# Performance work log

Hardware: AMD Instinct MI355X
Metric: run time of the kernel (lower is better)

## Reference

```python
import jax, jax.numpy as jnp
import numpy as np

B, T, C = 128, 256, 384
H, D = 6, 64

def setup_inputs() -> dict:
    key = jax.random.key(0)
    ks = jax.random.split(key, 6)
    s = 1.0 / np.sqrt(C)
    return {
        "x": jax.random.normal(ks[0], (B, T, C), dtype=jnp.float32),
        "Wq": jax.random.normal(ks[1], (H, C, D), dtype=jnp.float32) * s,
        "Wk": jax.random.normal(ks[2], (H, C, D), dtype=jnp.float32) * s,
        "Wv": jax.random.normal(ks[3], (H, C, D), dtype=jnp.float32) * s,
        "Wp": jax.random.normal(ks[4], (C, C), dtype=jnp.float32) * s,
        "bp": jnp.zeros((C,), dtype=jnp.float32),
    }

def reference(x, Wq, Wk, Wv, Wp, bp):
    # per-head projections (all heads at once): [B,T,C] x [H,C,D] -> [B,H,T,D]
    q = jnp.einsum("btc,hcd->bhtd", x, Wq)
    k = jnp.einsum("btc,hcd->bhtd", x, Wk)
    v = jnp.einsum("btc,hcd->bhtd", x, Wv)
    scale = 1.0 / jnp.sqrt(jnp.asarray(D, dtype=x.dtype))
    # scores [B,H,T,T], causal mask, softmax
    wei = jnp.einsum("bhqd,bhkd->bhqk", q, k) * scale
    causal = jnp.tril(jnp.ones((T, T), dtype=bool))
    wei = jnp.where(causal, wei, -jnp.inf)
    wei = jax.nn.softmax(wei, axis=-1)
    # dropout layers are identity in eval mode
    out = jnp.einsum("bhqk,bhkd->bhqd", wei, v)
    # concat heads: [B,T,H*D]
    out = out.transpose(0, 2, 1, 3).reshape(B, T, H * D)
    return out @ Wp + bp
```

## Files before the change

### kernel.cpp

```cpp
#include <hip/hip_runtime.h>
#include <stdint.h>


typedef __attribute__((ext_vector_type(8))) short bf16x8;
typedef __attribute__((ext_vector_type(4))) float f32x4;
typedef __attribute__((ext_vector_type(16))) float f32x16;

__device__ __forceinline__ unsigned short f2b(float f) {
    union { float f; unsigned int u; } v; v.f = f;
    unsigned int u = v.u + 0x7fffu + ((v.u >> 16) & 1u);
    return (unsigned short)(u >> 16);
}

__device__ __forceinline__ unsigned int pk2(float lo, float hi) {
    return (unsigned int)f2b(lo) | ((unsigned int)f2b(hi) << 16);
}

__device__ __forceinline__ uint32_t cvtpk(float lo, float hi) {
    uint32_t r;
    asm("v_cvt_pk_bf16_f32 %0, %1, %2" : "=v"(r) : "v"(lo), "v"(hi));
    return r;
}

__device__ __forceinline__ void gload_lds16(const void* g, void* lds) {
    auto gp = reinterpret_cast<const __attribute__((address_space(1))) uint32_t*>(
        reinterpret_cast<uintptr_t>(g));
    auto lp = reinterpret_cast<__attribute__((address_space(3))) uint32_t*>(
        reinterpret_cast<uintptr_t>(lds));
    __builtin_amdgcn_global_load_lds(gp, lp, 16, 0, 0);
}

#define SBAR0() __builtin_amdgcn_sched_barrier(0)


__global__ void cvt_w_kernel(const float* __restrict__ Wq, const float* __restrict__ Wk,
                             const float* __restrict__ Wv, const float* __restrict__ Wp,
                             unsigned short* __restrict__ wt, unsigned short* __restrict__ wpt) {
    int i = blockIdx.x * 256 + threadIdx.x;
    if (i >= 589824) return;
    if (i < 442368) {
        int j = i / 384, c = i - j * 384;
        int p = j / 384, rem = j - p * 384;
        int h = rem >> 6, d = rem & 63;
        const float* W = (p == 0) ? Wq : ((p == 1) ? Wk : Wv);
        wt[i] = f2b(W[(size_t)(h * 384 + c) * 64 + d]);
    } else {
        int i2 = i - 442368;
        int n = i2 / 384, c = i2 - n * 384;
        wpt[i2] = f2b(Wp[(size_t)c * 384 + n]);
    }
}


__global__ __launch_bounds__(256, 2) void gemm_qkv(
    const float* __restrict__ x,
    const unsigned short* __restrict__ wt,
    unsigned short* __restrict__ qO,
    unsigned short* __restrict__ kO,
    unsigned short* __restrict__ vO)
{
    extern __shared__ __align__(16) unsigned short smem[];
    float*          Af = (float*)smem;
    unsigned short* Bf = smem + 24576;

    const int tid  = threadIdx.x;
    const int lane = tid & 63;
    const int w    = tid >> 6;
    const int wm = w >> 1, wn = w & 1;

    const int flat = blockIdx.y * 9 + blockIdx.x;
    const int swz = (flat & 7) * 288 + (flat >> 3);
    const int bx = swz % 9, by = swz / 9;
    const int col0 = bx * 128;
    const int row0 = by * 128;

    const float* Abase = x + (size_t)row0 * 384;
    const unsigned short* Bbase = wt + (size_t)col0 * 384;

    f32x4 acc[4][4];
#pragma unroll
    for (int mf = 0; mf < 4; ++mf)
#pragma unroll
        for (int nf = 0; nf < 4; ++nf)
#pragma unroll
            for (int r = 0; r < 4; ++r) acc[mf][nf][r] = 0.f;

    const float* aSrc[4];
#pragma unroll
    for (int j = 0; j < 4; ++j) {
        const int ci = tid + 256 * j;
        aSrc[j] = Abase + (size_t)(ci >> 3) * 384 + ((ci & 7) ^ ((ci >> 3) & 7)) * 4;
    }
    const int bi0 = tid, bi1 = tid + 256;
    const unsigned short* bSrc0 = Bbase + (size_t)(bi0 >> 2) * 384 + ((bi0 & 3) ^ ((bi0 >> 3) & 3)) * 8;
    const unsigned short* bSrc1 = Bbase + (size_t)(bi1 >> 2) * 384 + ((bi1 & 3) ^ ((bi1 >> 3) & 3)) * 8;
    const int cb = w * 64;

    auto STAGE = [&](int buf, int kt) {
        const int k0_ = kt * 32;
#pragma unroll
        for (int j = 0; j < 4; ++j)
            gload_lds16(aSrc[j] + k0_, Af + buf * 4096 + (cb + 256 * j) * 4);
        gload_lds16(bSrc0 + k0_, Bf + buf * 4096 + (cb + 0) * 8);
        gload_lds16(bSrc1 + k0_, Bf + buf * 4096 + (cb + 256) * 8);
    };

    const int fr  = lane & 15;
    const int oc  = lane >> 4;
    const int qlA0 = (2 * oc)     ^ (fr & 7);
    const int qlA1 = (2 * oc + 1) ^ (fr & 7);
    const int ocB  = oc ^ ((fr >> 1) & 3);

    auto COMPUTE = [&](int buf) {
        const float* A = Af + buf * 4096;
        const unsigned short* B = Bf + buf * 4096;
        bf16x8 aF[4], bF[4];
#pragma unroll
        for (int mf = 0; mf < 4; ++mf) {
            const int rowA = wm * 64 + mf * 16 + fr;
            f32x4 F0 = *(const f32x4*)&A[rowA * 32 + qlA0 * 4];
            f32x4 F1 = *(const f32x4*)&A[rowA * 32 + qlA1 * 4];
            union { uint32_t u[4]; bf16x8 v; } pk;
            pk.u[0] = cvtpk(F0[0], F0[1]);
            pk.u[1] = cvtpk(F0[2], F0[3]);
            pk.u[2] = cvtpk(F1[0], F1[1]);
            pk.u[3] = cvtpk(F1[2], F1[3]);
            aF[mf] = pk.v;
        }
#pragma unroll
        for (int nf = 0; nf < 4; ++nf)
            bF[nf] = *(const bf16x8*)&B[(wn * 64 + nf * 16 + fr) * 32 + ocB * 8];
#pragma unroll
        for (int mf = 0; mf < 4; ++mf)
#pragma unroll
            for (int nf = 0; nf < 4; ++nf)
                acc[mf][nf] = __builtin_amdgcn_mfma_f32_16x16x32_bf16(aF[mf], bF[nf], acc[mf][nf], 0, 0, 0);
    };

    STAGE(0, 0);
    STAGE(1, 1);
    SBAR0();
    int bufS = 2, bufC = 0;
    for (int t = 0; t < 10; ++t) {
        STAGE(bufS, t + 2);
        bufS = (bufS == 2) ? 0 : bufS + 1;
        SBAR0();
        asm volatile("s_waitcnt vmcnt(12)" ::: "memory");
        SBAR0();
        __builtin_amdgcn_s_barrier();
        SBAR0();
        COMPUTE(bufC);
        bufC = (bufC == 2) ? 0 : bufC + 1;
        SBAR0();
        __builtin_amdgcn_s_barrier();
        SBAR0();
    }
    asm volatile("s_waitcnt vmcnt(6)" ::: "memory");
    SBAR0();
    __builtin_amdgcn_s_barrier();
    SBAR0();
    COMPUTE(1);
    SBAR0();
    __builtin_amdgcn_s_barrier();
    SBAR0();
    asm volatile("s_waitcnt vmcnt(0)" ::: "memory");
    SBAR0();
    __builtin_amdgcn_s_barrier();
    SBAR0();
    COMPUTE(2);
    __syncthreads();

    unsigned short* Ct = smem;
    const int co = tid & 15;
    const int rr = tid >> 4;
    const int colg = col0 + co * 8;
    const int p = colg / 384;
    const int rem = colg - p * 384;
    const int h = rem >> 6;
    const int d = rem & 63;
    unsigned short* dst = (p == 0) ? qO : ((p == 1) ? kO : vO);

#pragma unroll
    for (int ph = 0; ph < 2; ++ph) {
        if (wm == ph) {
#pragma unroll
            for (int mf = 0; mf < 4; ++mf)
#pragma unroll
                for (int nf = 0; nf < 4; ++nf)
#pragma unroll
                    for (int r = 0; r < 4; ++r)
                        Ct[(mf * 16 + (lane >> 4) * 4 + r) * 136 + wn * 64 + nf * 16 + (lane & 15)] =
                            f2b(acc[mf][nf][r]);
        }
        __syncthreads();
#pragma unroll
        for (int it = 0; it < 4; ++it) {
            const int r_loc = it * 16 + rr;
            const int m = row0 + ph * 64 + r_loc;
            const int b = m >> 8, t = m & 255;
            uint4 val = *(const uint4*)&Ct[r_loc * 136 + co * 8];
            *(uint4*)&dst[(size_t)((b * 6 + h) * 256 + t) * 64 + d] = val;
        }
        __syncthreads();
    }
}


__global__ __launch_bounds__(512, 4) void attn_kernel(
    const unsigned short* __restrict__ Qg,
    const unsigned short* __restrict__ Kg,
    const unsigned short* __restrict__ Vg,
    unsigned short* __restrict__ Og)
{
    extern __shared__ __align__(16) unsigned short asmem[];
    unsigned short* Ks = asmem;
    unsigned short* Vs = asmem + 256 * 72;
    unsigned short* Ot = asmem;
    const int bh = blockIdx.x;
    const int b = bh / 6, h = bh - b * 6;
    const int tid = threadIdx.x;
    const int lane = tid & 63;
    const int w = tid >> 6;
    const int lo = lane & 31, hi = lane >> 5;

    const unsigned short* kg = Kg + (size_t)bh * 256 * 64;
#pragma unroll
    for (int j = 0; j < 4; ++j) {
        int chunk = tid + 512 * j;
        int key = chunk >> 3, dc = (chunk & 7) * 8;
        *(uint4*)&Ks[key * 72 + dc] = *(const uint4*)&kg[key * 64 + dc];
    }
    {
        const unsigned short* vg = Vg + (size_t)bh * 256 * 64;
        uint32_t* Vs32 = (uint32_t*)Vs;
#pragma unroll
        for (int i = 0; i < 2; ++i) {
            int u = tid + 512 * i;
            int t2 = (u & 31) | ((u >> 8) << 5);
            int dm = (u >> 5) & 7;
            uint4 r0 = *(const uint4*)&vg[(2 * t2 + 0) * 64 + dm * 8];
            uint4 r1 = *(const uint4*)&vg[(2 * t2 + 1) * 64 + dm * 8];
            const unsigned short* e0 = (const unsigned short*)&r0;
            const unsigned short* e1 = (const unsigned short*)&r1;
#pragma unroll
            for (int j = 0; j < 8; ++j)
                Vs32[(dm * 8 + j) * 132 + t2] = (uint32_t)e0[j] | ((uint32_t)e1[j] << 16);
        }
    }
    __syncthreads();

    const int q0 = w * 32;
    const unsigned short* qg = Qg + (size_t)bh * 256 * 64 + (size_t)(q0 + lo) * 64 + hi * 8;
    bf16x8 qF[4];
#pragma unroll
    for (int dc = 0; dc < 4; ++dc) qF[dc] = *(const bf16x8*)(qg + dc * 16);

    float m = -1e30f, ssum = 0.f;
    f32x16 o0, o1;
#pragma unroll
    for (int r = 0; r < 16; ++r) { o0[r] = 0.f; o1[r] = 0.f; }

    for (int kt = 0; kt <= w; ++kt) {
        f32x16 s;
#pragma unroll
        for (int r = 0; r < 16; ++r) s[r] = 0.f;
#pragma unroll
        for (int dc = 0; dc < 4; ++dc) {
            bf16x8 aK = *(const bf16x8*)&Ks[(kt * 32 + lo) * 72 + dc * 16 + hi * 8];
            s = __builtin_amdgcn_mfma_f32_32x32x16_bf16(aK, qF[dc], s, 0, 0, 0);
        }
        float p[16];
        float pmax = -1e30f;
        const bool diag = (kt == w);
#pragma unroll
        for (int r = 0; r < 16; ++r) {
            float sv = s[r] * 0.125f;
            const int keyl = (r & 3) + 8 * (r >> 2) + 4 * hi;
            if (diag && keyl > lo) sv = -1e30f;
            p[r] = sv;
            pmax = fmaxf(pmax, sv);
        }
        pmax = fmaxf(pmax, __shfl_xor(pmax, 32, 64));
        const float mn = fmaxf(m, pmax);
        const float sf = __expf(m - mn);
        m = mn;
        ssum *= sf;
#pragma unroll
        for (int r = 0; r < 16; ++r) { o0[r] *= sf; o1[r] *= sf; }
        float rs = 0.f;
#pragma unroll
        for (int r = 0; r < 16; ++r) { p[r] = __expf(p[r] - m); rs += p[r]; }
        rs += __shfl_xor(rs, 32, 64);
        ssum += rs;

        union { unsigned short u[16]; bf16x8 v[2]; } P;
        {
            float recv[4];
#pragma unroll
            for (int j2 = 0; j2 < 4; ++j2) {
                float sendv = hi ? p[j2] : p[4 + j2];
                recv[j2] = __shfl_xor(sendv, 32, 64);
            }
#pragma unroll
            for (int i = 0; i < 4; ++i) P.u[i]     = f2b(hi ? recv[i] : p[i]);
#pragma unroll
            for (int i = 0; i < 4; ++i) P.u[4 + i] = f2b(hi ? p[4 + i] : recv[i]);
        }
        {
            float recv[4];
#pragma unroll
            for (int j2 = 0; j2 < 4; ++j2) {
                float sendv = hi ? p[8 + j2] : p[12 + j2];
                recv[j2] = __shfl_xor(sendv, 32, 64);
            }
#pragma unroll
            for (int i = 0; i < 4; ++i) P.u[8 + i]  = f2b(hi ? recv[i] : p[8 + i]);
#pragma unroll
            for (int i = 0; i < 4; ++i) P.u[12 + i] = f2b(hi ? p[12 + i] : recv[i]);
        }

#pragma unroll
        for (int kc = 0; kc < 2; ++kc) {
            bf16x8 aV0 = *(const bf16x8*)&Vs[lo * 264 + kt * 32 + kc * 16 + hi * 8];
            o0 = __builtin_amdgcn_mfma_f32_32x32x16_bf16(aV0, P.v[kc], o0, 0, 0, 0);
            bf16x8 aV1 = *(const bf16x8*)&Vs[(32 + lo) * 264 + kt * 32 + kc * 16 + hi * 8];
            o1 = __builtin_amdgcn_mfma_f32_32x32x16_bf16(aV1, P.v[kc], o1, 0, 0, 0);
        }
    }

    __syncthreads();
    const float inv = 1.f / ssum;
    {
        uint32_t* ot32 = (uint32_t*)&Ot[w * 32 * 72];
#pragma unroll
        for (int g = 0; g < 4; ++g) {
            const int dbase0 = 8 * g + 4 * hi;
            uint32_t w0 = pk2(o0[4 * g + 0] * inv, o0[4 * g + 1] * inv);
            uint32_t w1 = pk2(o0[4 * g + 2] * inv, o0[4 * g + 3] * inv);
            int dw = lo * 36 + (dbase0 >> 1);
            ot32[dw] = w0;
            ot32[dw + 1] = w1;
            uint32_t w2 = pk2(o1[4 * g + 0] * inv, o1[4 * g + 1] * inv);
            uint32_t w3 = pk2(o1[4 * g + 2] * inv, o1[4 * g + 3] * inv);
            int dw1 = lo * 36 + ((32 + dbase0) >> 1);
            ot32[dw1] = w2;
            ot32[dw1 + 1] = w3;
        }
    }
    __syncthreads();
    {
        const unsigned short* ot = &Ot[w * 32 * 72];
        const int q = lane >> 1;
        const int half = (lane & 1) * 32;
        unsigned short* og = Og + (size_t)(b * 256 + q0 + q) * 384 + h * 64 + half;
#pragma unroll
        for (int jj = 0; jj < 4; ++jj) {
            uint4 val = *(const uint4*)&ot[q * 72 + half + jj * 8];
            *(uint4*)&og[jj * 8] = val;
        }
    }
}


__global__ __launch_bounds__(256, 3) void gemm_proj(
    const unsigned short* __restrict__ ob,
    const unsigned short* __restrict__ wpt,
    const float* __restrict__ bp,
    float* __restrict__ out)
{
    __shared__ __align__(16) unsigned short As[3][128 * 32];
    __shared__ __align__(16) unsigned short Bs[3][128 * 32];
    const int tid  = threadIdx.x;
    const int lane = tid & 63;
    const int w    = tid >> 6;
    const int wm = w >> 1, wn = w & 1;

    const int flat = blockIdx.y * 3 + blockIdx.x;
    const int swz = (flat & 7) * 96 + (flat >> 3);
    const int bx = swz % 3, by = swz / 3;
    const int col0 = bx * 128;
    const int row0 = by * 128;

    const unsigned short* Abase = ob  + (size_t)row0 * 384;
    const unsigned short* Bbase = wpt + (size_t)col0 * 384;

    f32x4 acc[4][4];
#pragma unroll
    for (int mf = 0; mf < 4; ++mf)
#pragma unroll
        for (int nf = 0; nf < 4; ++nf)
#pragma unroll
            for (int r = 0; r < 4; ++r) acc[mf][nf][r] = 0.f;

    const int ci0 = tid;
    const int ci1 = tid + 256;
    const int r0c = ci0 >> 2, o0c = (ci0 & 3) ^ ((ci0 >> 3) & 3);
    const int r1c = ci1 >> 2, o1c = (ci1 & 3) ^ ((ci1 >> 3) & 3);
    const unsigned short* aSrc0 = Abase + (size_t)r0c * 384 + o0c * 8;
    const unsigned short* aSrc1 = Abase + (size_t)r1c * 384 + o1c * 8;
    const unsigned short* bSrc0 = Bbase + (size_t)r0c * 384 + o0c * 8;
    const unsigned short* bSrc1 = Bbase + (size_t)r1c * 384 + o1c * 8;
    const int cb = w * 64;

    auto STAGE = [&](int buf, int kt) {
        const int k0_ = kt * 32;
        gload_lds16(aSrc0 + k0_, (unsigned short*)As[buf] + (cb + 0) * 8);
        gload_lds16(bSrc0 + k0_, (unsigned short*)Bs[buf] + (cb + 0) * 8);
        gload_lds16(aSrc1 + k0_, (unsigned short*)As[buf] + (cb + 256) * 8);
        gload_lds16(bSrc1 + k0_, (unsigned short*)Bs[buf] + (cb + 256) * 8);
    };

    const int fr = lane & 15;
    const int oc = (lane >> 4) ^ ((fr >> 1) & 3);

    auto COMPUTE = [&](int buf) {
        const unsigned short* A = As[buf];
        const unsigned short* B = Bs[buf];
        bf16x8 aF[4], bF[4];
#pragma unroll
        for (int mf = 0; mf < 4; ++mf)
            aF[mf] = *(const bf16x8*)&A[(wm * 64 + mf * 16 + fr) * 32 + oc * 8];
#pragma unroll
        for (int nf = 0; nf < 4; ++nf)
            bF[nf] = *(const bf16x8*)&B[(wn * 64 + nf * 16 + fr) * 32 + oc * 8];
#pragma unroll
        for (int mf = 0; mf < 4; ++mf)
#pragma unroll
            for (int nf = 0; nf < 4; ++nf)
                acc[mf][nf] = __builtin_amdgcn_mfma_f32_16x16x32_bf16(aF[mf], bF[nf], acc[mf][nf], 0, 0, 0);
    };

    STAGE(0, 0);
    STAGE(1, 1);
    SBAR0();
    int bufS = 2, bufC = 0;
    for (int t = 0; t < 10; ++t) {
        STAGE(bufS, t + 2);
        bufS = (bufS == 2) ? 0 : bufS + 1;
        SBAR0();
        asm volatile("s_waitcnt vmcnt(8)" ::: "memory");
        SBAR0();
        __builtin_amdgcn_s_barrier();
        SBAR0();
        COMPUTE(bufC);
        bufC = (bufC == 2) ? 0 : bufC + 1;
        SBAR0();
        __builtin_amdgcn_s_barrier();
        SBAR0();
    }
    asm volatile("s_waitcnt vmcnt(4)" ::: "memory");
    SBAR0();
    __builtin_amdgcn_s_barrier();
    SBAR0();
    COMPUTE(1);
    SBAR0();
    __builtin_amdgcn_s_barrier();
    SBAR0();
    asm volatile("s_waitcnt vmcnt(0)" ::: "memory");
    SBAR0();
    __builtin_amdgcn_s_barrier();
    SBAR0();
    COMPUTE(2);

#pragma unroll
    for (int nf = 0; nf < 4; ++nf) {
        const int col = col0 + wn * 64 + nf * 16 + (lane & 15);
        const float bias = bp[col];
#pragma unroll
        for (int mf = 0; mf < 4; ++mf) {
            const int mbase = row0 + wm * 64 + mf * 16 + ((lane >> 4) * 4);
#pragma unroll
            for (int r = 0; r < 4; ++r) {
                const int mrow = mbase + r;
                out[(size_t)mrow * 384 + col] = acc[mf][nf][r] + bias;
            }
        }
    }
}


extern "C" void kernel_launch(void* const* d_in, const int* in_sizes, int n_in,
                              void* d_out, int out_size, void* d_ws, size_t ws_size,
                              hipStream_t stream) {
    const float* x  = (const float*)d_in[0];
    const float* Wq = (const float*)d_in[1];
    const float* Wk = (const float*)d_in[2];
    const float* Wv = (const float*)d_in[3];
    const float* Wp = (const float*)d_in[4];
    const float* bp = (const float*)d_in[5];
    float* out = (float*)d_out;

    char* ws = (char*)d_ws;
    unsigned short* ob  = (unsigned short*)(ws);
    unsigned short* qb  = (unsigned short*)(ws + 25165824);
    unsigned short* kb  = (unsigned short*)(ws + 50331648);
    unsigned short* vb  = (unsigned short*)(ws + 75497472);
    unsigned short* wt  = (unsigned short*)(ws + 100663296);
    unsigned short* wpt = (unsigned short*)(ws + 101548032);

    cvt_w_kernel<<<2304, 256, 0, stream>>>(Wq, Wk, Wv, Wp, wt, wpt);
    gemm_qkv<<<dim3(9, 256), 256, 73728, stream>>>(x, wt, qb, kb, vb);
    attn_kernel<<<768, 512, 70656, stream>>>(qb, kb, vb, ob);
    gemm_proj<<<dim3(3, 256), 256, 0, stream>>>(ob, wpt, bp, out);
}
```

Baseline: 109.6 us.

## Keep full bf16 x row-tile resident in LDS and loop over all N tiles in QKV GEMM

The QKV projection now gives each block a 128-row strip of x. The strip is converted to bf16 once into LDS (swizzled), and the block loops over all nine 128-column weight tiles, streaming only B through a triple buffer. This removes the repeated fp32 loads and conversions of x across nine column blocks, at the cost of 256 large-LDS blocks at one block per CU. The attention kernel also raises wave priority around its MFMA sections and skips the output rescale unless the running max grows by more than a threshold, which is an exact lazy-rescale trick.

```diff
diff --git a/kernel.cpp b/kernel.cpp
--- a/kernel.cpp
+++ b/kernel.cpp
@@ -52,7 +52,7 @@
 }
 
 
-__global__ __launch_bounds__(256, 2) void gemm_qkv(
+__global__ __launch_bounds__(512, 1) void gemm_qkv(
     const float* __restrict__ x,
     const unsigned short* __restrict__ wt,
     unsigned short* __restrict__ qO,
@@ -60,148 +60,140 @@
     unsigned short* __restrict__ vO)
 {
     extern __shared__ __align__(16) unsigned short smem[];
-    float*          Af = (float*)smem;
-    unsigned short* Bf = smem + 24576;
+    unsigned short* Afull = smem;
+    unsigned short* Bbuf  = smem + 49152;
+    unsigned short* Ct    = smem + 49152 + 12288;
 
     const int tid  = threadIdx.x;
     const int lane = tid & 63;
     const int w    = tid >> 6;
-    const int wm = w >> 1, wn = w & 1;
-
-    const int flat = blockIdx.y * 9 + blockIdx.x;
-    const int swz = (flat & 7) * 288 + (flat >> 3);
-    const int bx = swz % 9, by = swz / 9;
-    const int col0 = bx * 128;
-    const int row0 = by * 128;
-
-    const float* Abase = x + (size_t)row0 * 384;
-    const unsigned short* Bbase = wt + (size_t)col0 * 384;
-
-    f32x4 acc[4][4];
-#pragma unroll
-    for (int mf = 0; mf < 4; ++mf)
-#pragma unroll
-        for (int nf = 0; nf < 4; ++nf)
-#pragma unroll
-            for (int r = 0; r < 4; ++r) acc[mf][nf][r] = 0.f;
-
-    const float* aSrc[4];
-#pragma unroll
-    for (int j = 0; j < 4; ++j) {
-        const int ci = tid + 256 * j;
-        aSrc[j] = Abase + (size_t)(ci >> 3) * 384 + ((ci & 7) ^ ((ci >> 3) & 7)) * 4;
-    }
-    const int bi0 = tid, bi1 = tid + 256;
-    const unsigned short* bSrc0 = Bbase + (size_t)(bi0 >> 2) * 384 + ((bi0 & 3) ^ ((bi0 >> 3) & 3)) * 8;
-    const unsigned short* bSrc1 = Bbase + (size_t)(bi1 >> 2) * 384 + ((bi1 & 3) ^ ((bi1 >> 3) & 3)) * 8;
-    const int cb = w * 64;
-
-    auto STAGE = [&](int buf, int kt) {
-        const int k0_ = kt * 32;
-#pragma unroll
-        for (int j = 0; j < 4; ++j)
-            gload_lds16(aSrc[j] + k0_, Af + buf * 4096 + (cb + 256 * j) * 4);
-        gload_lds16(bSrc0 + k0_, Bf + buf * 4096 + (cb + 0) * 8);
-        gload_lds16(bSrc1 + k0_, Bf + buf * 4096 + (cb + 256) * 8);
-    };
+    const int wm   = w >> 1;
+    const int wn   = w & 1;
+    const int row0 = blockIdx.x * 128;
+
+#pragma unroll
+    for (int j = 0; j < 12; ++j) {
+        const int ci  = j * 512 + tid;
+        const int row = ci / 48;
+        const int og  = ci - row * 48;
+        const float* src = x + (size_t)(row0 + row) * 384 + og * 8;
+        float4 f0 = *(const float4*)src;
+        float4 f1 = *(const float4*)(src + 4);
+        uint4 wv;
+        wv.x = cvtpk(f0.x, f0.y); wv.y = cvtpk(f0.z, f0.w);
+        wv.z = cvtpk(f1.x, f1.y); wv.w = cvtpk(f1.z, f1.w);
+        const int ol = og ^ (row & 7);
+        *(uint4*)&Afull[row * 384 + ol * 8] = wv;
+    }
+
+    const int brow = tid >> 2;
+    const int bog  = (tid & 3) ^ ((tid >> 3) & 3);
+    const unsigned short* bSrcBase = wt + (size_t)brow * 384 + bog * 8;
 
     const int fr  = lane & 15;
-    const int oc  = lane >> 4;
-    const int qlA0 = (2 * oc)     ^ (fr & 7);
-    const int qlA1 = (2 * oc + 1) ^ (fr & 7);
-    const int ocB  = oc ^ ((fr >> 1) & 3);
-
-    auto COMPUTE = [&](int buf) {
-        const float* A = Af + buf * 4096;
-        const unsigned short* B = Bf + buf * 4096;
-        bf16x8 aF[4], bF[4];
-#pragma unroll
-        for (int mf = 0; mf < 4; ++mf) {
-            const int rowA = wm * 64 + mf * 16 + fr;
-            f32x4 F0 = *(const f32x4*)&A[rowA * 32 + qlA0 * 4];
-            f32x4 F1 = *(const f32x4*)&A[rowA * 32 + qlA1 * 4];
-            union { uint32_t u[4]; bf16x8 v; } pk;
-            pk.u[0] = cvtpk(F0[0], F0[1]);
-            pk.u[1] = cvtpk(F0[2], F0[3]);
-            pk.u[2] = cvtpk(F1[0], F1[1]);
-            pk.u[3] = cvtpk(F1[2], F1[3]);
-            aF[mf] = pk.v;
-        }
-#pragma unroll
-        for (int nf = 0; nf < 4; ++nf)
-            bF[nf] = *(const bf16x8*)&B[(wn * 64 + nf * 16 + fr) * 32 + ocB * 8];
-#pragma unroll
-        for (int mf = 0; mf < 4; ++mf)
+    const int q4  = lane >> 4;
+    const int ocB = q4 ^ ((fr >> 1) & 3);
+
+    __syncthreads();
+
+    for (int n = 0; n < 9; ++n) {
+        const unsigned short* bS = bSrcBase + (size_t)n * 49152;
+
+        f32x4 acc[2][4];
+#pragma unroll
+        for (int mf = 0; mf < 2; ++mf)
 #pragma unroll
             for (int nf = 0; nf < 4; ++nf)
-                acc[mf][nf] = __builtin_amdgcn_mfma_f32_16x16x32_bf16(aF[mf], bF[nf], acc[mf][nf], 0, 0, 0);
-    };
-
-    STAGE(0, 0);
-    STAGE(1, 1);
-    SBAR0();
-    int bufS = 2, bufC = 0;
-    for (int t = 0; t < 10; ++t) {
-        STAGE(bufS, t + 2);
-        bufS = (bufS == 2) ? 0 : bufS + 1;
-        SBAR0();
-        asm volatile("s_waitcnt vmcnt(12)" ::: "memory");
+#pragma unroll
+                for (int r = 0; r < 4; ++r) acc[mf][nf][r] = 0.f;
+
+        auto STAGE = [&](int buf, int kt) {
+            gload_lds16(bS + kt * 32, Bbuf + buf * 4096 + tid * 8);
+        };
+        auto COMPUTE = [&](int kt, int buf) {
+            const unsigned short* Bp = Bbuf + buf * 4096;
+            bf16x8 aF[2], bF[4];
+#pragma unroll
+            for (int mf = 0; mf < 2; ++mf) {
+                const int r  = wm * 32 + mf * 16 + fr;
+                const int ol = (kt * 4 + q4) ^ (r & 7);
+                aF[mf] = *(const bf16x8*)&Afull[r * 384 + ol * 8];
+            }
+#pragma unroll
+            for (int nf = 0; nf < 4; ++nf)
+                bF[nf] = *(const bf16x8*)&Bp[(wn * 64 + nf * 16 + fr) * 32 + ocB * 8];
+#pragma unroll
+            for (int mf = 0; mf < 2; ++mf)
+#pragma unroll
+                for (int nf = 0; nf < 4; ++nf)
+                    acc[mf][nf] = __builtin_amdgcn_mfma_f32_16x16x32_bf16(aF[mf], bF[nf], acc[mf][nf], 0, 0, 0);
+        };
+
+        STAGE(0, 0);
+        STAGE(1, 1);
+        SBAR0();
+        int bufS = 2, bufC = 0;
+        for (int kt = 0; kt < 10; ++kt) {
+            STAGE(bufS, kt + 2);
+            bufS = (bufS == 2) ? 0 : bufS + 1;
+            SBAR0();
+            asm volatile("s_waitcnt vmcnt(2)" ::: "memory");
+            SBAR0();
+            __builtin_amdgcn_s_barrier();
+            SBAR0();
+            COMPUTE(kt, bufC);
+            bufC = (bufC == 2) ? 0 : bufC + 1;
+            SBAR0();
+            __builtin_amdgcn_s_barrier();
+            SBAR0();
+        }
+        asm volatile("s_waitcnt vmcnt(1)" ::: "memory");
         SBAR0();
         __builtin_amdgcn_s_barrier();
         SBAR0();
-        COMPUTE(bufC);
-        bufC = (bufC == 2) ? 0 : bufC + 1;
+        COMPUTE(10, 1);
         SBAR0();
         __builtin_amdgcn_s_barrier();
         SBAR0();
-    }
-    asm volatile("s_waitcnt vmcnt(6)" ::: "memory");
-    SBAR0();
-    __builtin_amdgcn_s_barrier();
-    SBAR0();
-    COMPUTE(1);
-    SBAR0();
-    __builtin_amdgcn_s_barrier();
-    SBAR0();
-    asm volatile("s_waitcnt vmcnt(0)" ::: "memory");
-    SBAR0();
-    __builtin_amdgcn_s_barrier();
-    SBAR0();
-    COMPUTE(2);
-    __syncthreads();
-
-    unsigned short* Ct = smem;
-    const int co = tid & 15;
-    const int rr = tid >> 4;
-    const int colg = col0 + co * 8;
-    const int p = colg / 384;
-    const int rem = colg - p * 384;
-    const int h = rem >> 6;
-    const int d = rem & 63;
-    unsigned short* dst = (p == 0) ? qO : ((p == 1) ? kO : vO);
-
-#pragma unroll
-    for (int ph = 0; ph < 2; ++ph) {
-        if (wm == ph) {
-#pragma unroll
-            for (int mf = 0; mf < 4; ++mf)
-#pragma unroll
-                for (int nf = 0; nf < 4; ++nf)
-#pragma unroll
-                    for (int r = 0; r < 4; ++r)
-                        Ct[(mf * 16 + (lane >> 4) * 4 + r) * 136 + wn * 64 + nf * 16 + (lane & 15)] =
-                            f2b(acc[mf][nf][r]);
-        }
+        asm volatile("s_waitcnt vmcnt(0)" ::: "memory");
+        SBAR0();
+        __builtin_amdgcn_s_barrier();
+        SBAR0();
+        COMPUTE(11, 2);
         __syncthreads();
-#pragma unroll
-        for (int it = 0; it < 4; ++it) {
-            const int r_loc = it * 16 + rr;
-            const int m = row0 + ph * 64 + r_loc;
-            const int b = m >> 8, t = m & 255;
-            uint4 val = *(const uint4*)&Ct[r_loc * 136 + co * 8];
-            *(uint4*)&dst[(size_t)((b * 6 + h) * 256 + t) * 64 + d] = val;
-        }
-        __syncthreads();
+
+        const int co = tid & 15;
+        const int rr = tid >> 4;
+        const int colg = n * 128 + co * 8;
+        const int p = colg / 384;
+        const int rem = colg - p * 384;
+        const int h = rem >> 6;
+        const int d = rem & 63;
+        unsigned short* dst = (p == 0) ? qO : ((p == 1) ? kO : vO);
+
+#pragma unroll
+        for (int ph = 0; ph < 2; ++ph) {
+            if ((wm >> 1) == ph) {
+#pragma unroll
+                for (int mf = 0; mf < 2; ++mf)
+#pragma unroll
+                    for (int nf = 0; nf < 4; ++nf)
+#pragma unroll
+                        for (int r = 0; r < 4; ++r)
+                            Ct[((wm & 1) * 32 + mf * 16 + q4 * 4 + r) * 136 + wn * 64 + nf * 16 + fr] =
+                                f2b(acc[mf][nf][r]);
+            }
+            __syncthreads();
+#pragma unroll
+            for (int it = 0; it < 2; ++it) {
+                const int r_loc = it * 32 + rr;
+                const int m = row0 + ph * 64 + r_loc;
+                const int b = m >> 8, t = m & 255;
+                uint4 val = *(const uint4*)&Ct[r_loc * 136 + co * 8];
+                *(uint4*)&dst[(size_t)((b * 6 + h) * 256 + t) * 64 + d] = val;
+            }
+            __syncthreads();
+        }
     }
 }
 
@@ -264,11 +256,13 @@
         f32x16 s;
 #pragma unroll
         for (int r = 0; r < 16; ++r) s[r] = 0.f;
+        __builtin_amdgcn_s_setprio(1);
 #pragma unroll
         for (int dc = 0; dc < 4; ++dc) {
             bf16x8 aK = *(const bf16x8*)&Ks[(kt * 32 + lo) * 72 + dc * 16 + hi * 8];
             s = __builtin_amdgcn_mfma_f32_32x32x16_bf16(aK, qF[dc], s, 0, 0, 0);
         }
+        __builtin_amdgcn_s_setprio(0);
         float p[16];
         float pmax = -1e30f;
         const bool diag = (kt == w);
@@ -281,12 +275,13 @@
             pmax = fmaxf(pmax, sv);
         }
         pmax = fmaxf(pmax, __shfl_xor(pmax, 32, 64));
-        const float mn = fmaxf(m, pmax);
-        const float sf = __expf(m - mn);
-        m = mn;
-        ssum *= sf;
-#pragma unroll
-        for (int r = 0; r < 16; ++r) { o0[r] *= sf; o1[r] *= sf; }
+        if (pmax > m + 8.f) {
+            const float sf = __expf(m - pmax);
+            m = pmax;
+            ssum *= sf;
+#pragma unroll
+            for (int r = 0; r < 16; ++r) { o0[r] *= sf; o1[r] *= sf; }
+        }
         float rs = 0.f;
 #pragma unroll
         for (int r = 0; r < 16; ++r) { p[r] = __expf(p[r] - m); rs += p[r]; }
@@ -319,6 +314,7 @@
             for (int i = 0; i < 4; ++i) P.u[12 + i] = f2b(hi ? p[12 + i] : recv[i]);
         }
 
+        __builtin_amdgcn_s_setprio(1);
 #pragma unroll
         for (int kc = 0; kc < 2; ++kc) {
             bf16x8 aV0 = *(const bf16x8*)&Vs[lo * 264 + kt * 32 + kc * 16 + hi * 8];
@@ -326,6 +322,7 @@
             bf16x8 aV1 = *(const bf16x8*)&Vs[(32 + lo) * 264 + kt * 32 + kc * 16 + hi * 8];
             o1 = __builtin_amdgcn_mfma_f32_32x32x16_bf16(aV1, P.v[kc], o1, 0, 0, 0);
         }
+        __builtin_amdgcn_s_setprio(0);
     }
 
     __syncthreads();
@@ -499,7 +496,7 @@
     unsigned short* wpt = (unsigned short*)(ws + 101548032);
 
     cvt_w_kernel<<<2304, 256, 0, stream>>>(Wq, Wk, Wv, Wp, wt, wpt);
-    gemm_qkv<<<dim3(9, 256), 256, 73728, stream>>>(x, wt, qb, kb, vb);
+    gemm_qkv<<<256, 512, 140288, stream>>>(x, wt, qb, kb, vb);
     attn_kernel<<<768, 512, 70656, stream>>>(qb, kb, vb, ob);
     gemm_proj<<<dim3(3, 256), 256, 0, stream>>>(ob, wpt, bp, out);
 }
```

Measured after the change: 106.3 us. 3.0% less time.
